# Optimization experiments

Measured on AMD Instinct MI355X. Metric: run time of the kernel, lower is better.

Reference implementation:

```python
import jax, jax.numpy as jnp
import numpy as np

KS = 3      # kernel size
PAD = 1     # zero padding
STRIDE = 1
N = KS * KS # 9 sampling points per pixel


def _deform_conv(feature, offset, weight):
    """DeformConv2d: bilinear sample at learned offsets then 3x3 conv (no bias)."""
    b, c, h, w = feature.shape
    x = jnp.pad(feature, ((0, 0), (0, 0), (PAD, PAD), (PAD, PAD)))
    hp, wp = h + 2 * PAD, w + 2 * PAD
    dt = feature.dtype
    # p_n: kernel grid offsets, x(rows) first then y(cols) -> (2N,)
    rng = jnp.arange(-(KS - 1) // 2, (KS - 1) // 2 + 1, dtype=dt)
    pn_x, pn_y = jnp.meshgrid(rng, rng, indexing='ij')
    # p_0: base sampling grid starting at 1 (accounts for zero padding)
    p0_x, p0_y = jnp.meshgrid(jnp.arange(1, h + 1, dtype=dt),
                              jnp.arange(1, w + 1, dtype=dt), indexing='ij')
    # sampling locations p = p_0 + p_n + offset, split into x/y -> (b,h,w,N)
    off = jnp.transpose(offset, (0, 2, 3, 1))  # (b,h,w,2N)
    px = p0_x[None, :, :, None] + pn_x.reshape(-1)[None, None, None, :] + off[..., :N]
    py = p0_y[None, :, :, None] + pn_y.reshape(-1)[None, None, None, :] + off[..., N:]
    q_lt_x = jnp.clip(jnp.floor(px), 0, hp - 1)
    q_lt_y = jnp.clip(jnp.floor(py), 0, wp - 1)
    q_rb_x = jnp.clip(jnp.floor(px) + 1, 0, hp - 1)
    q_rb_y = jnp.clip(jnp.floor(py) + 1, 0, wp - 1)
    px = jnp.clip(px, 0, hp - 1)
    py = jnp.clip(py, 0, wp - 1)
    # bilinear weights for the 4 corners
    g_lt = (1 + (q_lt_x - px)) * (1 + (q_lt_y - py))
    g_rb = (1 - (q_rb_x - px)) * (1 - (q_rb_y - py))
    g_lb = (1 + (q_lt_x - px)) * (1 - (q_rb_y - py))
    g_rt = (1 - (q_rb_x - px)) * (1 + (q_lt_y - py))
    x_flat = x.reshape(b, c, hp * wp)

    def gather(qx, qy):
        idx = (qx * wp + qy).astype(jnp.int32).reshape(b, 1, -1)
        v = jnp.take_along_axis(x_flat, jnp.broadcast_to(idx, (b, c, h * w * N)), axis=2)
        return v.reshape(b, c, h, w, N)

    x_off = (g_lt[:, None] * gather(q_lt_x, q_lt_y)
             + g_rb[:, None] * gather(q_rb_x, q_rb_y)
             + g_lb[:, None] * gather(q_lt_x, q_rb_y)
             + g_rt[:, None] * gather(q_rb_x, q_lt_y))  # (b,c,h,w,N)
    # equivalent of _reshape_x_offset + conv(ks, stride=ks)
    x_off = x_off.reshape(b, c, h, w, KS, KS)
    return jnp.einsum('bchwij,ocij->bohw', x_off, weight)


def setup_inputs() -> dict:
    key = jax.random.key(0)
    k1, k2, k3 = jax.random.split(key, 3)
    B, C, H, W = 4, 256, 64, 64
    feature = jax.random.normal(k1, (B, C, H, W), dtype=jnp.float32)
    offset = jax.random.normal(k2, (B, 2 * N, H, W), dtype=jnp.float32)
    weight = jax.random.normal(k3, (C, C, KS, KS), dtype=jnp.float32) / np.sqrt(C * N)
    return {"feature": feature, "offset": offset, "weight": weight}


def reference(feature, offset, weight):
    f1 = jax.nn.relu(_deform_conv(feature, offset, weight))
    return jax.nn.relu(f1 + feature)
```

## Files before the change

### kernel.cpp

```cpp
#include <hip/hip_runtime.h>

#define HW    4096
#define J_TOT 16384
#define K_TOT 2304
#define C_CH  256

typedef unsigned short u16;
typedef unsigned int   u32;
typedef __attribute__((ext_vector_type(8))) short short8;
typedef __attribute__((ext_vector_type(4))) float f32x4;
typedef __attribute__((ext_vector_type(8))) unsigned short us8;

__device__ __forceinline__ float b2f(u16 u) { return __uint_as_float(((u32)u) << 16); }
__device__ __forceinline__ u16 f2b(float x) {
  u32 u = __float_as_uint(x);
  u += 0x7FFFu + ((u >> 16) & 1u);
  return (u16)(u >> 16);
}

__global__ void k_detect(const u16* __restrict__ f, int* __restrict__ flag) {
  __shared__ int sh[256];
  int t = threadIdx.x;
  int hits = 0;
  for (int i = t; i < 2048; i += 256) {
    u16 u = f[2 * i];
    int e = (u >> 7) & 0xFF;
    hits += (e >= 100 && e <= 141) ? 1 : 0;
  }
  sh[t] = hits;
  __syncthreads();
  if (t < 64) {
    int s = sh[t] + sh[t + 64] + sh[t + 128] + sh[t + 192];
#pragma unroll
    for (int off = 32; off > 0; off >>= 1) s += __shfl_down(s, off, 64);
    if (t == 0) flag[0] = (s > 1024) ? 1 : 0;
  }
}

__global__ __launch_bounds__(256) void k_prep(const void* __restrict__ featv,
                                              const void* __restrict__ wv,
                                              u16* __restrict__ ftr,
                                              u16* __restrict__ Wr,
                                              const int* __restrict__ flag) {
  int isbf = *flag;
  int bi = blockIdx.x;
  int t = threadIdx.x;
  if (bi < 4096) {
    __shared__ u16 tile[32][33];
    int b = bi >> 10;
    int y = (bi >> 7) & 7;
    int x = bi & 127;
    int hw0 = x << 5;
    int c0 = y << 5;
    int tx = t & 31, ty = t >> 5;
    if (isbf) {
      const u16* f = (const u16*)featv;
#pragma unroll
      for (int i = 0; i < 4; i++) {
        int c = c0 + ty + i * 8;
        tile[ty + i * 8][tx] = f[(((size_t)(b * C_CH + c)) << 12) + hw0 + tx];
      }
    } else {
      const float* f = (const float*)featv;
#pragma unroll
      for (int i = 0; i < 4; i++) {
        int c = c0 + ty + i * 8;
        tile[ty + i * 8][tx] = f2b(f[(((size_t)(b * C_CH + c)) << 12) + hw0 + tx]);
      }
    }
    __syncthreads();
#pragma unroll
    for (int i = 0; i < 4; i++) {
      int hw = hw0 + ty + i * 8;
      ftr[(((size_t)(b * HW + hw)) << 8) + c0 + tx] = tile[tx][ty + i * 8];
    }
  } else {
    int idx = (bi - 4096) * 256 + t;
    if (idx < C_CH * K_TOT) {
      int c = idx & 255;
      int n = (idx >> 8) % 9;
      int o = idx / K_TOT;
      int src = (o * 256 + c) * 9 + n;
      if (isbf) Wr[idx] = ((const u16*)wv)[src];
      else      Wr[idx] = f2b(((const float*)wv)[src]);
    }
  }
}

__global__ __launch_bounds__(512, 2) void k_fused(const u16* __restrict__ Wr,
                                                  const u16* __restrict__ ftr,
                                                  const void* __restrict__ offv,
                                                  const void* __restrict__ featv,
                                                  void* __restrict__ outv,
                                                  const int* __restrict__ flag) {
  __shared__ u16 Bs[2][64 * 256];
  __shared__ int   cidx[9][64][4];
  __shared__ float cgw[9][64][4];
  int isbf = *flag;
  int jb = blockIdx.x << 6;
  int b  = jb >> 12;
  int hw0 = jb & (HW - 1);
  int t = threadIdx.x;
  int wave = t >> 6, lane = t & 63;
  int lr = lane & 15, lk = lane >> 4;

  for (int task = t; task < 576; task += 512) {
    int px = task & 63, n = task >> 6;
    int phw = hw0 + px;
    int ph = phw >> 6, pw = phw & 63;
    size_t obi = (((size_t)(b * 18 + n)) << 12) + phw;
    float ox, oy;
    if (isbf) {
      const u16* po = (const u16*)offv;
      ox = b2f(po[obi]);
      oy = b2f(po[obi + (9u << 12)]);
    } else {
      const float* po = (const float*)offv;
      ox = po[obi];
      oy = po[obi + (9u << 12)];
    }
    int ki = n / 3, kj = n % 3;
    float sx = (float)(ph + ki) + ox;
    float sy = (float)(pw + kj) + oy;
    float fx = floorf(sx), fy = floorf(sy);
    float qltx = fminf(fmaxf(fx, 0.f), 65.f);
    float qlty = fminf(fmaxf(fy, 0.f), 65.f);
    float qrbx = fminf(fmaxf(fx + 1.f, 0.f), 65.f);
    float qrby = fminf(fmaxf(fy + 1.f, 0.f), 65.f);
    float pcx = fminf(fmaxf(sx, 0.f), 65.f);
    float pcy = fminf(fmaxf(sy, 0.f), 65.f);
    float dltx = 1.f + (qltx - pcx);
    float drbx = 1.f - (qrbx - pcx);
    float dlty = 1.f + (qlty - pcy);
    float drby = 1.f - (qrby - pcy);
    float g0 = dltx * dlty;
    float g1 = drbx * drby;
    float g2 = dltx * drby;
    float g3 = drbx * dlty;
    int x0 = (int)qltx, y0 = (int)qlty, x1 = (int)qrbx, y1 = (int)qrby;
    int v0 = (x0 >= 1 && x0 <= 64 && y0 >= 1 && y0 <= 64);
    int v1 = (x1 >= 1 && x1 <= 64 && y1 >= 1 && y1 <= 64);
    int v2 = (x0 >= 1 && x0 <= 64 && y1 >= 1 && y1 <= 64);
    int v3 = (x1 >= 1 && x1 <= 64 && y0 >= 1 && y0 <= 64);
    int base = b << 12;
    cidx[n][px][0] = v0 ? ((base + ((x0 - 1) << 6) + (y0 - 1)) << 8) : 0;
    cidx[n][px][1] = v1 ? ((base + ((x1 - 1) << 6) + (y1 - 1)) << 8) : 0;
    cidx[n][px][2] = v2 ? ((base + ((x0 - 1) << 6) + (y1 - 1)) << 8) : 0;
    cidx[n][px][3] = v3 ? ((base + ((x1 - 1) << 6) + (y0 - 1)) << 8) : 0;
    cgw[n][px][0] = v0 ? g0 : 0.f;
    cgw[n][px][1] = v1 ? g1 : 0.f;
    cgw[n][px][2] = v2 ? g2 : 0.f;
    cgw[n][px][3] = v3 ? g3 : 0.f;
  }

  f32x4 acc[4][4];
  f32x4 zero = {0.f, 0.f, 0.f, 0.f};
#pragma unroll
  for (int i = 0; i < 4; i++)
#pragma unroll
    for (int j = 0; j < 4; j++) acc[i][j] = zero;

  int pt = t - 256;
  int lane16 = pt & 15, grp = pt >> 4;
  const u16* aw = Wr + (size_t)(wave * 64 + lr) * K_TOT + lk * 8;

  for (int it = 0; it < 10; it++) {
    __syncthreads();
    if (wave >= 4) {
      if (it < 9) {
        int n = it;
        u16* dstp = Bs[it & 1];
#pragma unroll
        for (int s = 0; s < 4; s++) {
          int px = grp + s * 16;
          int i0 = cidx[n][px][0], i1 = cidx[n][px][1];
          int i2 = cidx[n][px][2], i3 = cidx[n][px][3];
          float g0 = cgw[n][px][0], g1 = cgw[n][px][1];
          float g2 = cgw[n][px][2], g3 = cgw[n][px][3];
#pragma unroll
          for (int half = 0; half < 2; half++) {
            int c16 = half * 16 + lane16;
            int ch = c16 * 8;
            us8 r0 = *(const us8*)(ftr + i0 + ch);
            us8 r1 = *(const us8*)(ftr + i1 + ch);
            us8 r2 = *(const us8*)(ftr + i2 + ch);
            us8 r3 = *(const us8*)(ftr + i3 + ch);
            us8 ov;
#pragma unroll
            for (int i = 0; i < 8; i++) {
              float v = g0 * b2f(r0[i]) + g1 * b2f(r1[i]) + g2 * b2f(r2[i]) + g3 * b2f(r3[i]);
              ov[i] = f2b(v);
            }
            int cs = c16 ^ (px & 7);
            *(us8*)(&dstp[px * 256 + cs * 8]) = ov;
          }
        }
      }
    } else {
      if (it > 0) {
        int m = it - 1;
        const u16* srcp = Bs[m & 1];
        const u16* an = aw + (m << 8);
#pragma unroll
        for (int kh = 0; kh < 2; kh++) {
          short8 A[4][4];
#pragma unroll
          for (int oi = 0; oi < 4; oi++)
#pragma unroll
            for (int k2 = 0; k2 < 4; k2++)
              A[oi][k2] = *(const short8*)(an + (size_t)oi * 16 * K_TOT + (kh * 4 + k2) * 32);
#pragma unroll
          for (int k2 = 0; k2 < 4; k2++) {
            int kc = kh * 4 + k2;
            short8 bf[4];
#pragma unroll
            for (int ji = 0; ji < 4; ji++) {
              int row = ji * 16 + lr;
              int cs = (kc * 4 + lk) ^ (lr & 7);
              bf[ji] = *(const short8*)(&srcp[row * 256 + cs * 8]);
            }
#pragma unroll
            for (int oi = 0; oi < 4; oi++)
#pragma unroll
              for (int ji = 0; ji < 4; ji++)
                acc[oi][ji] = __builtin_amdgcn_mfma_f32_16x16x32_bf16(A[oi][k2], bf[ji], acc[oi][ji], 0, 0, 0);
          }
        }
      }
    }
  }

  if (wave < 4) {
#pragma unroll
    for (int oi = 0; oi < 4; oi++) {
#pragma unroll
      for (int ji = 0; ji < 4; ji++) {
        int j = jb + ji * 16 + lr;
        int hww = j & (HW - 1);
        int o0 = wave * 64 + oi * 16 + lk * 4;
#pragma unroll
        for (int r = 0; r < 4; r++) {
          size_t oidx = (((size_t)(b * C_CH + o0 + r)) << 12) + hww;
          float v = acc[oi][ji][r];
          v = fmaxf(v, 0.f);
          float ft = isbf ? b2f(((const u16*)featv)[oidx]) : ((const float*)featv)[oidx];
          v = fmaxf(v + ft, 0.f);
          if (isbf) ((u16*)outv)[oidx] = f2b(v);
          else      ((float*)outv)[oidx] = v;
        }
      }
    }
  }
}

extern "C" void kernel_launch(void* const* d_in, const int* in_sizes, int n_in,
                              void* d_out, int out_size, void* d_ws, size_t ws_size,
                              hipStream_t stream) {
  const void* feat = d_in[0];
  const void* offs = d_in[1];
  const void* wght = d_in[2];

  const size_t off_flag = 0;
  const size_t off_wr   = 256;
  const size_t off_ftr  = off_wr + (size_t)1179648;
  const size_t need     = off_ftr + (size_t)8388608;
  if (ws_size < need) return;

  char* ws = (char*)d_ws;
  int* flag = (int*)(ws + off_flag);
  u16* Wr   = (u16*)(ws + off_wr);
  u16* ftr  = (u16*)(ws + off_ftr);

  k_detect<<<1, 256, 0, stream>>>((const u16*)feat, flag);
  k_prep<<<4096 + 2304, 256, 0, stream>>>(feat, wght, ftr, Wr, flag);
  k_fused<<<J_TOT / 64, 512, 0, stream>>>(Wr, ftr, offs, feat, d_out, flag);
}
```

Measured before the change: 153.3 us.

## Replace producer/consumer wave split with all-wave software-pipelined gather and MFMA

The fused kernel no longer splits waves into gather producers and MFMA consumers. All 8 waves now gather and interpolate the next kernel tap while running MFMAs on the current tap, and each wave covers 32 output channels instead of 64. Corner indices are stored as u16 in shared memory, and interpolation uses packed bf16 conversion. The separate dtype-detection kernel is dropped and detection is redone inside every block, which removes one launch but adds redundant global reads and an atomic per block.

After: 155.2 us. No clear change (+1.2%).

```diff
diff --git a/kernel.cpp b/kernel.cpp
--- a/kernel.cpp
+++ b/kernel.cpp
@@ -1,4 +1,5 @@
 #include <hip/hip_runtime.h>
+#include <hip/hip_bf16.h>
 
 #define HW    4096
 #define J_TOT 16384
@@ -10,6 +11,7 @@
 typedef __attribute__((ext_vector_type(8))) short short8;
 typedef __attribute__((ext_vector_type(4))) float f32x4;
 typedef __attribute__((ext_vector_type(8))) unsigned short us8;
+typedef __attribute__((ext_vector_type(4))) unsigned short us4;
 
 __device__ __forceinline__ float b2f(u16 u) { return __uint_as_float(((u32)u) << 16); }
 __device__ __forceinline__ u16 f2b(float x) {
@@ -17,36 +19,53 @@
   u += 0x7FFFu + ((u >> 16) & 1u);
   return (u16)(u >> 16);
 }
-
-__global__ void k_detect(const u16* __restrict__ f, int* __restrict__ flag) {
-  __shared__ int sh[256];
-  int t = threadIdx.x;
+__device__ __forceinline__ float blo(u32 u) { return __uint_as_float(u << 16); }
+__device__ __forceinline__ float bhi(u32 u) { return __uint_as_float(u & 0xFFFF0000u); }
+
+__device__ __forceinline__ us8 interp8(us8 r0, us8 r1, us8 r2, us8 r3,
+                                       float g0, float g1, float g2, float g3) {
+  us8 o;
+  const u32* p0 = (const u32*)&r0;
+  const u32* p1 = (const u32*)&r1;
+  const u32* p2 = (const u32*)&r2;
+  const u32* p3 = (const u32*)&r3;
+  u32* po = (u32*)&o;
+#pragma unroll
+  for (int i = 0; i < 4; i++) {
+    u32 a = p0[i], b = p1[i], c = p2[i], d = p3[i];
+    float2 v;
+    v.x = g0 * blo(a) + g1 * blo(b) + g2 * blo(c) + g3 * blo(d);
+    v.y = g0 * bhi(a) + g1 * bhi(b) + g2 * bhi(c) + g3 * bhi(d);
+    __hip_bfloat162 pk = __float22bfloat162_rn(v);
+    po[i] = *reinterpret_cast<u32*>(&pk);
+  }
+  return o;
+}
+
+__device__ __forceinline__ int detect_bf16(const u16* f, int t, int nthr, int* cnt) {
+  if (t == 0) *cnt = 0;
+  __syncthreads();
   int hits = 0;
-  for (int i = t; i < 2048; i += 256) {
+  for (int i = t; i < 2048; i += nthr) {
     u16 u = f[2 * i];
     int e = (u >> 7) & 0xFF;
     hits += (e >= 100 && e <= 141) ? 1 : 0;
   }
-  sh[t] = hits;
-  __syncthreads();
-  if (t < 64) {
-    int s = sh[t] + sh[t + 64] + sh[t + 128] + sh[t + 192];
-#pragma unroll
-    for (int off = 32; off > 0; off >>= 1) s += __shfl_down(s, off, 64);
-    if (t == 0) flag[0] = (s > 1024) ? 1 : 0;
-  }
+  atomicAdd(cnt, hits);
+  __syncthreads();
+  return (*cnt > 1024) ? 1 : 0;
 }
 
 __global__ __launch_bounds__(256) void k_prep(const void* __restrict__ featv,
                                               const void* __restrict__ wv,
                                               u16* __restrict__ ftr,
-                                              u16* __restrict__ Wr,
-                                              const int* __restrict__ flag) {
-  int isbf = *flag;
+                                              u16* __restrict__ Wr) {
+  __shared__ int cnt;
+  __shared__ u16 tile[32][33];
+  int t = threadIdx.x;
+  int isbf = detect_bf16((const u16*)featv, t, 256, &cnt);
   int bi = blockIdx.x;
-  int t = threadIdx.x;
   if (bi < 4096) {
-    __shared__ u16 tile[32][33];
     int b = bi >> 10;
     int y = (bi >> 7) & 7;
     int x = bi & 127;
@@ -76,33 +95,33 @@
     }
   } else {
     int idx = (bi - 4096) * 256 + t;
-    if (idx < C_CH * K_TOT) {
-      int c = idx & 255;
-      int n = (idx >> 8) % 9;
-      int o = idx / K_TOT;
-      int src = (o * 256 + c) * 9 + n;
-      if (isbf) Wr[idx] = ((const u16*)wv)[src];
-      else      Wr[idx] = f2b(((const float*)wv)[src]);
-    }
-  }
-}
-
-__global__ __launch_bounds__(512, 2) void k_fused(const u16* __restrict__ Wr,
-                                                  const u16* __restrict__ ftr,
-                                                  const void* __restrict__ offv,
-                                                  const void* __restrict__ featv,
-                                                  void* __restrict__ outv,
-                                                  const int* __restrict__ flag) {
+    int c = idx & 255;
+    int n = (idx >> 8) % 9;
+    int o = idx / K_TOT;
+    int src = (o * 256 + c) * 9 + n;
+    if (isbf) Wr[idx] = ((const u16*)wv)[src];
+    else      Wr[idx] = f2b(((const float*)wv)[src]);
+  }
+}
+
+__global__ __launch_bounds__(512) void k_fused(const u16* __restrict__ Wr,
+                                               const u16* __restrict__ ftr,
+                                               const void* __restrict__ offv,
+                                               const void* __restrict__ featv,
+                                               void* __restrict__ outv) {
   __shared__ u16 Bs[2][64 * 256];
-  __shared__ int   cidx[9][64][4];
-  __shared__ float cgw[9][64][4];
-  int isbf = *flag;
+  __shared__ u16 cq[9][64][4];
+  __shared__ float cg[9][64][4];
+  __shared__ int cnt;
+  int t = threadIdx.x;
+  int isbf = detect_bf16((const u16*)featv, t, 512, &cnt);
+
   int jb = blockIdx.x << 6;
   int b  = jb >> 12;
   int hw0 = jb & (HW - 1);
-  int t = threadIdx.x;
   int wave = t >> 6, lane = t & 63;
   int lr = lane & 15, lk = lane >> 4;
+  int lane16 = t & 15, grp16 = t >> 4;
 
   for (int task = t; task < 576; task += 512) {
     int px = task & 63, n = task >> 6;
@@ -142,112 +161,110 @@
     int v1 = (x1 >= 1 && x1 <= 64 && y1 >= 1 && y1 <= 64);
     int v2 = (x0 >= 1 && x0 <= 64 && y1 >= 1 && y1 <= 64);
     int v3 = (x1 >= 1 && x1 <= 64 && y0 >= 1 && y0 <= 64);
-    int base = b << 12;
-    cidx[n][px][0] = v0 ? ((base + ((x0 - 1) << 6) + (y0 - 1)) << 8) : 0;
-    cidx[n][px][1] = v1 ? ((base + ((x1 - 1) << 6) + (y1 - 1)) << 8) : 0;
-    cidx[n][px][2] = v2 ? ((base + ((x0 - 1) << 6) + (y1 - 1)) << 8) : 0;
-    cidx[n][px][3] = v3 ? ((base + ((x1 - 1) << 6) + (y0 - 1)) << 8) : 0;
-    cgw[n][px][0] = v0 ? g0 : 0.f;
-    cgw[n][px][1] = v1 ? g1 : 0.f;
-    cgw[n][px][2] = v2 ? g2 : 0.f;
-    cgw[n][px][3] = v3 ? g3 : 0.f;
-  }
-
-  f32x4 acc[4][4];
+    cq[n][px][0] = v0 ? (u16)(((x0 - 1) << 6) + (y0 - 1)) : (u16)0;
+    cq[n][px][1] = v1 ? (u16)(((x1 - 1) << 6) + (y1 - 1)) : (u16)0;
+    cq[n][px][2] = v2 ? (u16)(((x0 - 1) << 6) + (y1 - 1)) : (u16)0;
+    cq[n][px][3] = v3 ? (u16)(((x1 - 1) << 6) + (y0 - 1)) : (u16)0;
+    cg[n][px][0] = v0 ? g0 : 0.f;
+    cg[n][px][1] = v1 ? g1 : 0.f;
+    cg[n][px][2] = v2 ? g2 : 0.f;
+    cg[n][px][3] = v3 ? g3 : 0.f;
+  }
+
+  f32x4 acc[2][4];
   f32x4 zero = {0.f, 0.f, 0.f, 0.f};
 #pragma unroll
-  for (int i = 0; i < 4; i++)
+  for (int i = 0; i < 2; i++)
 #pragma unroll
     for (int j = 0; j < 4; j++) acc[i][j] = zero;
 
-  int pt = t - 256;
-  int lane16 = pt & 15, grp = pt >> 4;
-  const u16* aw = Wr + (size_t)(wave * 64 + lr) * K_TOT + lk * 8;
-
-  for (int it = 0; it < 10; it++) {
+  const u16* awp[2];
+  awp[0] = Wr + (size_t)(wave * 32 + lr) * K_TOT + lk * 8;
+  awp[1] = awp[0] + (size_t)16 * K_TOT;
+
+  int bbase = b << 12;
+
+  us8 P[2][4];
+
+  auto loadGroup = [&](int n1, int g) {
+#pragma unroll
+    for (int u = 0; u < 2; u++) {
+      int px = grp16 + g * 32;
+      int c16 = u * 16 + lane16;
+      int ch = c16 * 8;
+      us4 q = *(const us4*)&cq[n1][px][0];
+      P[u][0] = *(const us8*)(ftr + ((bbase + q.x) << 8) + ch);
+      P[u][1] = *(const us8*)(ftr + ((bbase + q.y) << 8) + ch);
+      P[u][2] = *(const us8*)(ftr + ((bbase + q.z) << 8) + ch);
+      P[u][3] = *(const us8*)(ftr + ((bbase + q.w) << 8) + ch);
+    }
+  };
+  auto interpGroup = [&](int n1, int g, u16* dstp) {
+#pragma unroll
+    for (int u = 0; u < 2; u++) {
+      int px = grp16 + g * 32;
+      int c16 = u * 16 + lane16;
+      float4 g4 = *(const float4*)&cg[n1][px][0];
+      us8 ov = interp8(P[u][0], P[u][1], P[u][2], P[u][3], g4.x, g4.y, g4.z, g4.w);
+      int cs = c16 ^ (px & 7);
+      *(us8*)(&Bs[(n1) & 1][px * 256 + cs * 8]) = ov;
+      (void)dstp;
+    }
+  };
+  auto consume4 = [&](int n, int kc0) {
+    const u16* srcp = Bs[n & 1];
+#pragma unroll
+    for (int k2 = 0; k2 < 4; k2++) {
+      int kc = kc0 + k2;
+      short8 Af[2], Bf[4];
+#pragma unroll
+      for (int oi = 0; oi < 2; oi++)
+        Af[oi] = *(const short8*)(awp[oi] + (n << 8) + kc * 32);
+#pragma unroll
+      for (int ji = 0; ji < 4; ji++) {
+        int row = ji * 16 + lr;
+        int cs = (kc * 4 + lk) ^ (row & 7);
+        Bf[ji] = *(const short8*)(&srcp[row * 256 + cs * 8]);
+      }
+#pragma unroll
+      for (int oi = 0; oi < 2; oi++)
+#pragma unroll
+        for (int ji = 0; ji < 4; ji++)
+          acc[oi][ji] = __builtin_amdgcn_mfma_f32_16x16x32_bf16(Af[oi], Bf[ji], acc[oi][ji], 0, 0, 0);
+    }
+  };
+
+  __syncthreads();
+
+  loadGroup(0, 0); interpGroup(0, 0, nullptr);
+  loadGroup(0, 1); interpGroup(0, 1, nullptr);
+  __syncthreads();
+
+  for (int n = 0; n < 9; n++) {
+    if (n < 8) loadGroup(n + 1, 0);
+    consume4(n, 0);
+    if (n < 8) { interpGroup(n + 1, 0, nullptr); loadGroup(n + 1, 1); }
+    consume4(n, 4);
+    if (n < 8) interpGroup(n + 1, 1, nullptr);
     __syncthreads();
-    if (wave >= 4) {
-      if (it < 9) {
-        int n = it;
-        u16* dstp = Bs[it & 1];
-#pragma unroll
-        for (int s = 0; s < 4; s++) {
-          int px = grp + s * 16;
-          int i0 = cidx[n][px][0], i1 = cidx[n][px][1];
-          int i2 = cidx[n][px][2], i3 = cidx[n][px][3];
-          float g0 = cgw[n][px][0], g1 = cgw[n][px][1];
-          float g2 = cgw[n][px][2], g3 = cgw[n][px][3];
-#pragma unroll
-          for (int half = 0; half < 2; half++) {
-            int c16 = half * 16 + lane16;
-            int ch = c16 * 8;
-            us8 r0 = *(const us8*)(ftr + i0 + ch);
-            us8 r1 = *(const us8*)(ftr + i1 + ch);
-            us8 r2 = *(const us8*)(ftr + i2 + ch);
-            us8 r3 = *(const us8*)(ftr + i3 + ch);
-            us8 ov;
-#pragma unroll
-            for (int i = 0; i < 8; i++) {
-              float v = g0 * b2f(r0[i]) + g1 * b2f(r1[i]) + g2 * b2f(r2[i]) + g3 * b2f(r3[i]);
-              ov[i] = f2b(v);
-            }
-            int cs = c16 ^ (px & 7);
-            *(us8*)(&dstp[px * 256 + cs * 8]) = ov;
-          }
-        }
-      }
-    } else {
-      if (it > 0) {
-        int m = it - 1;
-        const u16* srcp = Bs[m & 1];
-        const u16* an = aw + (m << 8);
-#pragma unroll
-        for (int kh = 0; kh < 2; kh++) {
-          short8 A[4][4];
-#pragma unroll
-          for (int oi = 0; oi < 4; oi++)
-#pragma unroll
-            for (int k2 = 0; k2 < 4; k2++)
-              A[oi][k2] = *(const short8*)(an + (size_t)oi * 16 * K_TOT + (kh * 4 + k2) * 32);
-#pragma unroll
-          for (int k2 = 0; k2 < 4; k2++) {
-            int kc = kh * 4 + k2;
-            short8 bf[4];
-#pragma unroll
-            for (int ji = 0; ji < 4; ji++) {
-              int row = ji * 16 + lr;
-              int cs = (kc * 4 + lk) ^ (lr & 7);
-              bf[ji] = *(const short8*)(&srcp[row * 256 + cs * 8]);
-            }
-#pragma unroll
-            for (int oi = 0; oi < 4; oi++)
-#pragma unroll
-              for (int ji = 0; ji < 4; ji++)
-                acc[oi][ji] = __builtin_amdgcn_mfma_f32_16x16x32_bf16(A[oi][k2], bf[ji], acc[oi][ji], 0, 0, 0);
-          }
-        }
-      }
-    }
-  }
-
-  if (wave < 4) {
-#pragma unroll
-    for (int oi = 0; oi < 4; oi++) {
-#pragma unroll
-      for (int ji = 0; ji < 4; ji++) {
-        int j = jb + ji * 16 + lr;
-        int hww = j & (HW - 1);
-        int o0 = wave * 64 + oi * 16 + lk * 4;
-#pragma unroll
-        for (int r = 0; r < 4; r++) {
-          size_t oidx = (((size_t)(b * C_CH + o0 + r)) << 12) + hww;
-          float v = acc[oi][ji][r];
-          v = fmaxf(v, 0.f);
-          float ft = isbf ? b2f(((const u16*)featv)[oidx]) : ((const float*)featv)[oidx];
-          v = fmaxf(v + ft, 0.f);
-          if (isbf) ((u16*)outv)[oidx] = f2b(v);
-          else      ((float*)outv)[oidx] = v;
-        }
+  }
+
+#pragma unroll
+  for (int oi = 0; oi < 2; oi++) {
+#pragma unroll
+    for (int ji = 0; ji < 4; ji++) {
+      int j = jb + ji * 16 + lr;
+      int hww = j & (HW - 1);
+      int o0 = wave * 32 + oi * 16 + lk * 4;
+#pragma unroll
+      for (int r = 0; r < 4; r++) {
+        size_t oidx = (((size_t)(b * C_CH + o0 + r)) << 12) + hww;
+        float v = acc[oi][ji][r];
+        v = fmaxf(v, 0.f);
+        float ft = isbf ? b2f(((const u16*)featv)[oidx]) : ((const float*)featv)[oidx];
+        v = fmaxf(v + ft, 0.f);
+        if (isbf) ((u16*)outv)[oidx] = f2b(v);
+        else      ((float*)outv)[oidx] = v;
       }
     }
   }
@@ -260,18 +277,15 @@
   const void* offs = d_in[1];
   const void* wght = d_in[2];
 
-  const size_t off_flag = 0;
-  const size_t off_wr   = 256;
+  const size_t off_wr   = 0;
   const size_t off_ftr  = off_wr + (size_t)1179648;
   const size_t need     = off_ftr + (size_t)8388608;
   if (ws_size < need) return;
 
   char* ws = (char*)d_ws;
-  int* flag = (int*)(ws + off_flag);
   u16* Wr   = (u16*)(ws + off_wr);
   u16* ftr  = (u16*)(ws + off_ftr);
 
-  k_detect<<<1, 256, 0, stream>>>((const u16*)feat, flag);
-  k_prep<<<4096 + 2304, 256, 0, stream>>>(feat, wght, ftr, Wr, flag);
-  k_fused<<<J_TOT / 64, 512, 0, stream>>>(Wr, ftr, offs, feat, d_out, flag);
-}
+  k_prep<<<4096 + 2304, 256, 0, stream>>>(feat, wght, ftr, Wr);
+  k_fused<<<J_TOT / 64, 512, 0, stream>>>(Wr, ftr, offs, feat, d_out);
+}
```
